# Kernel tuning notes

Hardware: AMD Instinct MI355X
Metric: run time of the kernel (lower is better)

## Reference

```python
import jax, jax.numpy as jnp
import numpy as np

B, D, F_UP, F_DOWN, C = 4096, 768, 12288, 12288, 256


def setup_inputs() -> dict:
    key = jax.random.key(0)
    ks = jax.random.split(key, 12)
    s = np.float32(1.0 / np.sqrt(D))
    return {
        'initial_acts': jax.random.normal(ks[0], (B, D), jnp.float32),
        'x_up': jax.random.normal(ks[1], (B, D), jnp.float32),
        'ln_scale': jax.random.uniform(ks[2], (B,), jnp.float32) + 0.5,
        'W_enc_up': jax.random.normal(ks[3], (F_UP, D), jnp.float32) * s,
        'b_enc_up': jax.random.normal(ks[4], (F_UP,), jnp.float32) * 0.01,
        'b_dec_up': jax.random.normal(ks[5], (D,), jnp.float32) * 0.01,
        'W_dec_up': jax.random.normal(ks[6], (D, F_UP), jnp.float32) * s,
        'W_enc_down': jax.random.normal(ks[7], (F_DOWN, D), jnp.float32) * s,
        'b_enc_down': jax.random.normal(ks[8], (F_DOWN,), jnp.float32) * 0.01,
        'b_dec_down': jax.random.normal(ks[9], (D,), jnp.float32) * 0.01,
        'W_dec_down': jax.random.normal(ks[10], (D, F_DOWN), jnp.float32) * s,
        'connections': jax.random.randint(ks[11], (F_DOWN, C), 0, F_UP, jnp.int64),
        'k_up': 64,
        'k_down': 64,
    }


def _topk_sparse(pre, k):
    # pre: [B, F] -> keep top-k per row, zeros elsewhere
    vals, idx = jax.lax.top_k(pre, k)
    rows = jnp.arange(pre.shape[0])[:, None]
    return jnp.zeros_like(pre).at[rows, idx].set(vals)


def _topk_encode(x, W_enc, b_enc, b_dec, k):
    # AutoEncoderTopK.encode: relu(encoder(x - b_dec)), then top-k sparsify
    pre = jax.nn.relu((x - b_dec) @ W_enc.T + b_enc)
    return _topk_sparse(pre, k)


def reference(initial_acts, x_up, ln_scale, W_enc_up, b_enc_up, b_dec_up,
              W_dec_up, W_enc_down, b_enc_down, b_dec_down, W_dec_down,
              connections, k_up, k_down):
    f_down, f_up = W_enc_down.shape[0], W_enc_up.shape[0]
    # upstream features (vanilla_forward -> features[up_name])
    feat_up = _topk_encode(x_up, W_enc_up, b_enc_up, b_dec_up, k_up)  # [B, F_up]
    # connection mask [F_down, F_up] from index tensor
    rows = jnp.arange(f_down)[:, None]
    mask = jnp.zeros((f_down, f_up), jnp.bool_).at[rows, connections].set(True)
    # get_pruned_contributions: masked virtual-weight matmul
    virtual_w = (W_enc_down @ W_dec_up) * mask                        # [F_down, F_up]
    contributions = feat_up @ virtual_w.T + (W_enc_down @ b_dec_up)   # [B, F_down]
    # get_initial_contributions + accumulate
    approx = initial_acts @ W_enc_down.T + contributions
    # layernorm scale, encoder bias, b_dec correction
    approx = approx / ln_scale[:, None] + b_enc_down - (W_enc_down @ b_dec_down)
    # downstream TopK + decode
    feat_down = _topk_sparse(approx, k_down)                          # [B, F_down]
    recon = feat_down @ W_dec_down.T + b_dec_down                     # [B, D]
    return recon
```

## Files before the change

kernel.cpp:

```cpp
#include <hip/hip_runtime.h>
#include <stdint.h>

#define B_    4096
#define D_    768
#define FUP   12288
#define FDN   12288
#define CONN  256
#define KTOP  64
#define CHUNK 1024
#define NCH   (B_ / CHUNK)
#define CH2   512
#define NCH2  (B_ / CH2)
#define PDW   1024
#define NPW   (FUP / PDW)

typedef short short8v __attribute__((ext_vector_type(8)));
typedef float f32x4  __attribute__((ext_vector_type(4)));


__device__ __forceinline__ unsigned fkey(float x) {
    unsigned u = __float_as_uint(x);
    return (u & 0x80000000u) ? ~u : (u | 0x80000000u);
}

__device__ void topk64_block(const float* vals, int n, int* gidx, float* gval,
                             unsigned* hist, int* scratch)
{
    const int tid = threadIdx.x;
    if (tid == 0) { scratch[0] = KTOP; scratch[1] = 0; scratch[2] = 0; scratch[3] = 0; }
    for (int l = 24; l >= 0; l -= 8) {
        hist[tid] = 0;
        __syncthreads();
        unsigned prefix = (unsigned)scratch[1];
        unsigned hm = (l == 24) ? 0u : (0xFFFFFFFFu << (l + 8));
        for (int i = tid; i < n; i += 256) {
            unsigned key = fkey(vals[i]);
            if ((key & hm) == (prefix & hm)) atomicAdd(&hist[(key >> l) & 255], 1u);
        }
        __syncthreads();
        if (tid == 0) {
            int need = scratch[0];
            unsigned acc = 0;
            for (int b2 = 255; b2 >= 0; --b2) {
                unsigned h = hist[b2];
                if (acc + h >= (unsigned)need) {
                    scratch[1] = (int)(prefix | ((unsigned)b2 << l));
                    scratch[0] = need - (int)acc;
                    break;
                }
                acc += h;
            }
        }
        __syncthreads();
    }
    unsigned thresh = (unsigned)scratch[1];
    for (int i = tid; i < n; i += 256) {
        float v = vals[i];
        unsigned key = fkey(v);
        if (key > thresh) {
            int p = atomicAdd(&scratch[2], 1);
            gidx[p] = i; gval[p] = v;
        } else if (key == thresh) {
            int p = atomicAdd(&scratch[3], 1);
            if (p < 64) scratch[4 + p] = i;
        }
    }
    __syncthreads();
    if (tid == 0) {
        int cnt = scratch[2];
        int ne  = KTOP - cnt;
        int ec  = scratch[3] < 64 ? scratch[3] : 64;
        for (int a2 = 0; a2 < ne; ++a2) {
            int best = 0x7fffffff, bi = -1;
            for (int q = 0; q < ec; ++q) {
                int id = scratch[4 + q];
                if (id >= 0 && id < best) { best = id; bi = q; }
            }
            if (bi >= 0) {
                scratch[4 + bi] = -1;
                gidx[cnt + a2] = best; gval[cnt + a2] = vals[best];
            }
        }
    }
    __syncthreads();
}


__global__ void k_detect(const int* __restrict__ conn, int* mode) {
    if (blockIdx.x == 0 && threadIdx.x == 0) {
        int z = 1;
        for (int i = 1; i < 128; i += 2) z &= (conn[i] == 0);
        *mode = z;
    }
}

__device__ __forceinline__ int getconn(const int* c, size_t e, int mode) {
    return mode ? c[2 * e] : c[e];
}

__global__ void k_zero(unsigned* __restrict__ p, int n) {
    for (int i = blockIdx.x * blockDim.x + threadIdx.x; i < n;
         i += gridDim.x * blockDim.x)
        p[i] = 0u;
}

__global__ void k_transpose(const float* __restrict__ in, float* __restrict__ out,
                            int R, int Cc) {
    __shared__ float t[32][33];
    int x = blockIdx.x * 32 + threadIdx.x;
    int yb = blockIdx.y * 32;
    for (int j = threadIdx.y; j < 32; j += 8)
        t[j][threadIdx.x] = in[(size_t)(yb + j) * Cc + x];
    __syncthreads();
    int xo  = yb + threadIdx.x;
    int yb2 = blockIdx.x * 32;
    for (int j = threadIdx.y; j < 32; j += 8)
        out[(size_t)(yb2 + j) * R + xo] = t[threadIdx.x][j];
}

__global__ void k_precompute(const float* __restrict__ Wup, const float* __restrict__ Wdn,
                             const float* __restrict__ b_enc_up, const float* __restrict__ b_enc_down,
                             const float* __restrict__ b_dec_up, const float* __restrict__ b_dec_down,
                             float* __restrict__ bias_up, float* __restrict__ c_in,
                             float* __restrict__ c_out) {
    int wave = threadIdx.x >> 6, lane = threadIdx.x & 63;
    int f = blockIdx.x * 4 + wave;
    if (f >= FUP) return;
    const float* ru = Wup + (size_t)f * D_;
    const float* rd = Wdn + (size_t)f * D_;
    float s1 = 0.f, s2 = 0.f, s3 = 0.f;
    for (int d = lane; d < D_; d += 64) {
        float bu = b_dec_up[d], bd = b_dec_down[d];
        s1 += ru[d] * bu;
        float w = rd[d];
        s2 += w * bu;
        s3 += w * bd;
    }
    for (int m = 32; m; m >>= 1) {
        s1 += __shfl_xor(s1, m);
        s2 += __shfl_xor(s2, m);
        s3 += __shfl_xor(s3, m);
    }
    if (!lane) {
        bias_up[f] = b_enc_up[f] - s1;
        c_in[f]  = s2;
        c_out[f] = b_enc_down[f] - s3;
    }
}

__device__ __forceinline__ unsigned short bf16rne(float f) {
    unsigned u = __float_as_uint(f);
    unsigned r = u + 0x7FFFu + ((u >> 16) & 1u);
    return (unsigned short)(r >> 16);
}
__global__ __launch_bounds__(256) void k_split3(const float* __restrict__ in,
                                                unsigned short* __restrict__ out,
                                                int R) {
    const size_t plane = (size_t)R * D_;
    size_t base = ((size_t)blockIdx.x * 256 + threadIdx.x) * 8;
    float v[8];
    *(float4*)&v[0] = *(const float4*)(in + base);
    *(float4*)&v[4] = *(const float4*)(in + base + 4);
    unsigned short h[8], m[8], l[8];
#pragma unroll
    for (int i = 0; i < 8; ++i) {
        float f = v[i];
        unsigned short hb = bf16rne(f);
        float hf = __uint_as_float((unsigned)hb << 16);
        float r1 = f - hf;
        unsigned short mb = bf16rne(r1);
        float mf = __uint_as_float((unsigned)mb << 16);
        float r2 = r1 - mf;
        unsigned short lb = bf16rne(r2);
        h[i] = hb; m[i] = mb; l[i] = lb;
    }
    *(short8v*)(out + base)             = *(short8v*)h;
    *(short8v*)(out + plane + base)     = *(short8v*)m;
    *(short8v*)(out + 2 * plane + base) = *(short8v*)l;
}

#define GBM 128
#define GBN 128
#define GBK 32
#define LDK 40
__global__ __launch_bounds__(256, 2) void k_gemm_mfma(
    const unsigned short* __restrict__ Asp, const unsigned short* __restrict__ Bsp,
    float* __restrict__ C, const float* __restrict__ bias,
    int M, int N, int doRelu)
{
    __shared__ __attribute__((aligned(16))) unsigned short Al[3][GBM][LDK];
    __shared__ __attribute__((aligned(16))) unsigned short Bl[3][GBN][LDK];
    const int tid = threadIdx.x;
    const int bm = blockIdx.y * GBM, bn = blockIdx.x * GBN;
    const int wid = tid >> 6, lane = tid & 63;
    const int wm = (wid >> 1) * 64, wn = (wid & 1) * 64;
    const int l15 = lane & 15, lk8 = (lane >> 4) * 8;
    const size_t psA = (size_t)M * D_, psB = (size_t)N * D_;
    f32x4 acc[4][4] = {};
    for (int k0 = 0; k0 < D_; k0 += GBK) {
        __syncthreads();
#pragma unroll
        for (int t = 0; t < 6; ++t) {
            int id = t * 256 + tid;
            int p = id / 512, rem = id & 511;
            int r = rem >> 2, c4 = rem & 3;
            *(short8v*)&Al[p][r][c4 * 8] =
                *(const short8v*)(Asp + p * psA + (size_t)(bm + r) * D_ + k0 + c4 * 8);
            *(short8v*)&Bl[p][r][c4 * 8] =
                *(const short8v*)(Bsp + p * psB + (size_t)(bn + r) * D_ + k0 + c4 * 8);
        }
        __syncthreads();
        short8v af[3][4], bf[3][4];
#pragma unroll
        for (int i = 0; i < 4; ++i) {
#pragma unroll
            for (int p = 0; p < 3; ++p) {
                af[p][i] = *(const short8v*)&Al[p][wm + i * 16 + l15][lk8];
                bf[p][i] = *(const short8v*)&Bl[p][wn + i * 16 + l15][lk8];
            }
        }
#pragma unroll
        for (int i = 0; i < 4; ++i)
#pragma unroll
            for (int j = 0; j < 4; ++j) {
                acc[i][j] = __builtin_amdgcn_mfma_f32_16x16x32_bf16(af[0][i], bf[0][j], acc[i][j], 0, 0, 0);
                acc[i][j] = __builtin_amdgcn_mfma_f32_16x16x32_bf16(af[0][i], bf[1][j], acc[i][j], 0, 0, 0);
                acc[i][j] = __builtin_amdgcn_mfma_f32_16x16x32_bf16(af[1][i], bf[0][j], acc[i][j], 0, 0, 0);
                acc[i][j] = __builtin_amdgcn_mfma_f32_16x16x32_bf16(af[1][i], bf[1][j], acc[i][j], 0, 0, 0);
                acc[i][j] = __builtin_amdgcn_mfma_f32_16x16x32_bf16(af[0][i], bf[2][j], acc[i][j], 0, 0, 0);
                acc[i][j] = __builtin_amdgcn_mfma_f32_16x16x32_bf16(af[2][i], bf[0][j], acc[i][j], 0, 0, 0);
            }
    }
#pragma unroll
    for (int i = 0; i < 4; ++i) {
        int gr0 = bm + wm + i * 16 + (lane >> 4) * 4;
#pragma unroll
        for (int j = 0; j < 4; ++j) {
            int gc = bn + wn + j * 16 + l15;
            float bv = bias ? bias[gc] : 0.f;
#pragma unroll
            for (int q = 0; q < 4; ++q) {
                float v = acc[i][j][q] + bv;
                if (doRelu) v = fmaxf(v, 0.f);
                C[(size_t)(gr0 + q) * N + gc] = v;
            }
        }
    }
}

__global__ __launch_bounds__(256) void k_topk_up(const float* __restrict__ big,
                                                 int* __restrict__ up_idx,
                                                 float* __restrict__ up_val) {
    __shared__ __attribute__((aligned(16))) float row[FUP];
    __shared__ unsigned hist[256];
    __shared__ int scratch[68];
    int b = blockIdx.x;
    const float4* s4 = (const float4*)(big + (size_t)b * FUP);
    float4* r4 = (float4*)row;
    for (int i = threadIdx.x; i < FUP / 4; i += 256) r4[i] = s4[i];
    __syncthreads();
    topk64_block(row, FUP, up_idx + b * 64, up_val + b * 64, hist, scratch);
}

__global__ __launch_bounds__(256) void k_sortwin(
    const int* __restrict__ conn, const int* __restrict__ mode_p,
    unsigned short* __restrict__ ent_fu, unsigned char* __restrict__ ent_c,
    unsigned short* __restrict__ woff)
{
    __shared__ int crow[CONN];
    __shared__ int cnt[NPW + 1];
    __shared__ int base[NPW + 1];
    __shared__ int cur[NPW + 1];
    int fd = blockIdx.x, tid = threadIdx.x;
    int mode = *mode_p;
    crow[tid] = getconn(conn, (size_t)fd * CONN + tid, mode);
    if (tid <= NPW) cnt[tid] = 0;
    __syncthreads();
    int fu = crow[tid];
    bool dup = false;
    for (int q = 0; q < tid; ++q) dup |= (crow[q] == fu);
    int win = dup ? NPW : (fu / PDW);
    atomicAdd(&cnt[win], 1);
    __syncthreads();
    if (tid == 0) {
        int run = 0;
        for (int i = 0; i <= NPW; ++i) { base[i] = run; run += cnt[i]; }
    }
    __syncthreads();
    if (tid <= NPW) {
        woff[fd * (NPW + 2) + tid] = (unsigned short)base[tid];
        cur[tid] = base[tid];
    }
    if (tid == 0) woff[fd * (NPW + 2) + NPW + 1] = (unsigned short)CONN;
    __syncthreads();
    int pos = atomicAdd(&cur[win], 1);
    ent_fu[(size_t)fd * CONN + pos] = (unsigned short)fu;
    ent_c[(size_t)fd * CONN + pos]  = (unsigned char)tid;
}

__global__ __launch_bounds__(256) void k_pd2(
    const float* __restrict__ Wdn, const float* __restrict__ WduT,
    const unsigned short* __restrict__ ent_fu, const unsigned char* __restrict__ ent_c,
    const unsigned short* __restrict__ woff, float* __restrict__ pd)
{
    __shared__ __attribute__((aligned(16))) float wrow[D_];
    int fd = blockIdx.x, win = blockIdx.y, tid = threadIdx.x;
    int s = woff[fd * (NPW + 2) + win];
    int e = woff[fd * (NPW + 2) + win + 1];
    if (win == NPW) {
        for (int t = s + tid; t < e; t += 256)
            pd[(size_t)fd * CONN + ent_c[(size_t)fd * CONN + t]] = 0.f;
        return;
    }
    if (s == e) return;
    const float4* wsrc = (const float4*)(Wdn + (size_t)fd * D_);
    for (int i = tid; i < D_ / 4; i += 256) ((float4*)wrow)[i] = wsrc[i];
    __syncthreads();
    const int wave = tid >> 6, lane = tid & 63;
    const int grp = lane >> 4, gi = lane & 15;
    float4 wr[12];
#pragma unroll
    for (int j = 0; j < 12; ++j)
        wr[j] = *(const float4*)&wrow[gi * 4 + j * 64];
    for (int q = s + wave * 4; q < e; q += 16) {
        int idx = q + grp;
        bool act = idx < e;
        int idxc = act ? idx : (e - 1);
        int fu = ent_fu[(size_t)fd * CONN + idxc];
        const float* wu = WduT + (size_t)fu * D_;
        float sacc = 0.f;
#pragma unroll
        for (int j = 0; j < 12; ++j) {
            float4 u = *(const float4*)&wu[gi * 4 + j * 64];
            sacc = fmaf(u.x, wr[j].x, sacc);
            sacc = fmaf(u.y, wr[j].y, sacc);
            sacc = fmaf(u.z, wr[j].z, sacc);
            sacc = fmaf(u.w, wr[j].w, sacc);
        }
#pragma unroll
        for (int m = 1; m < 16; m <<= 1) sacc += __shfl_xor(sacc, m);
        if (act && gi == 0)
            pd[(size_t)fd * CONN + ent_c[(size_t)fd * CONN + idx]] = sacc;
    }
}

__global__ void k_hist(const int* __restrict__ conn, const int* __restrict__ mode_p,
                       unsigned* __restrict__ counts, int total) {
    int mode = *mode_p;
    for (int e = blockIdx.x * blockDim.x + threadIdx.x; e < total;
         e += gridDim.x * blockDim.x)
        atomicAdd(&counts[getconn(conn, (size_t)e, mode)], 1u);
}

__global__ void k_scan(const unsigned* __restrict__ counts,
                       unsigned* __restrict__ offsets, unsigned* __restrict__ cursor) {
    __shared__ unsigned sums[256];
    int tid = threadIdx.x;
    const int CH = FUP / 256;
    unsigned local = 0;
    for (int i = 0; i < CH; ++i) local += counts[tid * CH + i];
    sums[tid] = local;
    __syncthreads();
    for (int off = 1; off < 256; off <<= 1) {
        unsigned v = 0;
        if (tid >= off) v = sums[tid - off];
        __syncthreads();
        sums[tid] += v;
        __syncthreads();
    }
    unsigned run = (tid == 0) ? 0u : sums[tid - 1];
    for (int i = 0; i < CH; ++i) {
        int idx = tid * CH + i;
        offsets[idx] = run;
        cursor[idx]  = run;
        run += counts[idx];
    }
    if (tid == 255) offsets[FUP] = run;
}

__global__ void k_scatter(const int* __restrict__ conn, const int* __restrict__ mode_p,
                          const float* __restrict__ pd, unsigned* __restrict__ cursor,
                          unsigned short* __restrict__ rev_fd, float* __restrict__ rev_w,
                          int total) {
    int mode = *mode_p;
    for (int e = blockIdx.x * blockDim.x + threadIdx.x; e < total;
         e += gridDim.x * blockDim.x) {
        int fu = getconn(conn, (size_t)e, mode);
        unsigned pos = atomicAdd(&cursor[fu], 1u);
        rev_fd[pos] = (unsigned short)(e >> 8);
        rev_w[pos]  = pd[e];
    }
}

__global__ __launch_bounds__(256) void k_down(
    const float* __restrict__ big , const float* __restrict__ ln_scale,
    const float* __restrict__ c_in, const float* __restrict__ c_out,
    const int* __restrict__ up_idx, const float* __restrict__ up_val,
    const unsigned* __restrict__ offsets, const unsigned short* __restrict__ rev_fd,
    const float* __restrict__ rev_w, int* __restrict__ down_idx,
    float* __restrict__ down_val)
{
    __shared__ __attribute__((aligned(16))) float contrib[FDN];
    __shared__ unsigned hist[256];
    __shared__ int scratch[68];
    int b = blockIdx.x, tid = threadIdx.x;
    float4* c4 = (float4*)contrib;
    for (int i = tid; i < FDN / 4; i += 256) c4[i] = make_float4(0.f, 0.f, 0.f, 0.f);
    __syncthreads();
    for (int j = 0; j < KTOP; ++j) {
        int fu = up_idx[b * 64 + j];
        float v = up_val[b * 64 + j];
        unsigned s = offsets[fu], e = offsets[fu + 1];
        for (unsigned t = s + tid; t < e; t += 256)
            atomicAdd(&contrib[rev_fd[t]], v * rev_w[t]);
    }
    __syncthreads();
    float ls = ln_scale[b];
    const float* ap = big + (size_t)b * FDN;
    for (int i = tid; i < FDN; i += 256)
        contrib[i] = (ap[i] + contrib[i] + c_in[i]) / ls + c_out[i];
    __syncthreads();
    topk64_block(contrib, FDN, down_idx + b * 64, down_val + b * 64, hist, scratch);
}

__global__ __launch_bounds__(256) void k_decode(
    const int* __restrict__ down_idx, const float* __restrict__ down_val,
    const float* __restrict__ WddT, const float* __restrict__ b_dec_down,
    float* __restrict__ out)
{
    __shared__ int fidx[64];
    __shared__ float fval[64];
    int b = blockIdx.x, tid = threadIdx.x;
    if (tid < 64) { fidx[tid] = down_idx[b * 64 + tid]; fval[tid] = down_val[b * 64 + tid]; }
    __syncthreads();
    float a0 = b_dec_down[tid], a1 = b_dec_down[tid + 256], a2 = b_dec_down[tid + 512];
    for (int j = 0; j < 64; ++j) {
        const float* r = WddT + (size_t)fidx[j] * D_;
        float v = fval[j];
        a0 += v * r[tid];
        a1 += v * r[tid + 256];
        a2 += v * r[tid + 512];
    }
    float* o = out + (size_t)b * D_;
    o[tid] = a0; o[tid + 256] = a1; o[tid + 512] = a2;
}


extern "C" void kernel_launch(void* const* d_in, const int* in_sizes, int n_in,
                              void* d_out, int out_size, void* d_ws, size_t ws_size,
                              hipStream_t stream)
{
    const float* initial_acts = (const float*)d_in[0];
    const float* x_up         = (const float*)d_in[1];
    const float* ln_scale     = (const float*)d_in[2];
    const float* W_enc_up     = (const float*)d_in[3];
    const float* b_enc_up     = (const float*)d_in[4];
    const float* b_dec_up     = (const float*)d_in[5];
    const float* W_dec_up     = (const float*)d_in[6];
    const float* W_enc_down   = (const float*)d_in[7];
    const float* b_enc_down   = (const float*)d_in[8];
    const float* b_dec_down   = (const float*)d_in[9];
    const float* W_dec_down   = (const float*)d_in[10];
    const int*   conn         = (const int*)d_in[11];
    float* out = (float*)d_out;

    char* w = (char*)d_ws;
    float*          big      = (float*)(w);
    float*          pd       = (float*)(w);
    unsigned short* ent_fu   = (unsigned short*)(w + 12582912);
    unsigned char*  ent_c    = (unsigned char*) (w + 18874368);
    unsigned short* woff     = (unsigned short*)(w + 22020096);
    unsigned short* Bsplit   = (unsigned short*)(w + 50331648);
    float*          Wt       = (float*)(w + 50331648);
    float*          rev_w    = (float*)(w + 106954752);
    unsigned short* Asplit1  = (unsigned short*)(w + 106954752);
    unsigned short* rev_fd   = (unsigned short*)(w + 119537664);
    unsigned short* Asplit2  = (unsigned short*)(w + 125829120);
    int*            up_idx   = (int*)  (w + 128188416);
    float*          up_val   = (float*)(w + 129236992);
    int*            down_idx = (int*)  (w + 130285568);
    float*          down_val = (float*)(w + 131334144);
    unsigned*       offsets  = (unsigned*)(w + 132382720);
    unsigned*       cursor   = (unsigned*)(w + 132448256);
    unsigned*       counts   = (unsigned*)(w + 132513792);
    float*          bias_up  = (float*)(w + 132579328);
    float*          c_in     = (float*)(w + 132628480);
    float*          c_out    = (float*)(w + 132677632);
    int*            mode_p   = (int*)  (w + 132726784);

    const int total_conn = FDN * CONN;
    dim3 tb(32, 8);

    k_detect<<<1, 64, 0, stream>>>(conn, mode_p);
    k_precompute<<<FUP / 4, 256, 0, stream>>>(W_enc_up, W_enc_down, b_enc_up, b_enc_down,
                                              b_dec_up, b_dec_down, bias_up, c_in, c_out);
    k_split3<<<FUP * D_ / 2048, 256, 0, stream>>>(W_enc_up, Bsplit, FUP);
    for (int c = 0; c < NCH; ++c) {
        k_split3<<<CHUNK * D_ / 2048, 256, 0, stream>>>(x_up + (size_t)c * CHUNK * D_,
                                                        Asplit1, CHUNK);
        k_gemm_mfma<<<dim3(FUP / GBN, CHUNK / GBM), 256, 0, stream>>>(
            Asplit1, Bsplit, big, bias_up, CHUNK, FUP, 1);
        k_topk_up<<<CHUNK, 256, 0, stream>>>(big, up_idx + (size_t)c * CHUNK * 64,
                                             up_val + (size_t)c * CHUNK * 64);
    }
    k_transpose<<<dim3(FUP / 32, D_ / 32), tb, 0, stream>>>(W_dec_up, Wt, D_, FUP);
    k_sortwin<<<FDN, 256, 0, stream>>>(conn, mode_p, ent_fu, ent_c, woff);
    k_pd2<<<dim3(FDN, NPW + 1), 256, 0, stream>>>(W_enc_down, Wt, ent_fu, ent_c, woff, pd);
    k_zero<<<48, 256, 0, stream>>>(counts, FUP);
    k_hist<<<4096, 256, 0, stream>>>(conn, mode_p, counts, total_conn);
    k_scan<<<1, 256, 0, stream>>>(counts, offsets, cursor);
    k_scatter<<<4096, 256, 0, stream>>>(conn, mode_p, pd, cursor, rev_fd, rev_w, total_conn);
    k_split3<<<FDN * D_ / 2048, 256, 0, stream>>>(W_enc_down, Bsplit, FDN);
    for (int c = 0; c < NCH2; ++c) {
        k_split3<<<CH2 * D_ / 2048, 256, 0, stream>>>(initial_acts + (size_t)c * CH2 * D_,
                                                      Asplit2, CH2);
        k_gemm_mfma<<<dim3(FDN / GBN, CH2 / GBM), 256, 0, stream>>>(
            Asplit2, Bsplit, big, nullptr, CH2, FDN, 0);
        k_down<<<CH2, 256, 0, stream>>>(big, ln_scale + (size_t)c * CH2, c_in, c_out,
                                        up_idx + (size_t)c * CH2 * 64,
                                        up_val + (size_t)c * CH2 * 64,
                                        offsets, rev_fd, rev_w,
                                        down_idx + (size_t)c * CH2 * 64,
                                        down_val + (size_t)c * CH2 * 64);
    }
    k_transpose<<<dim3(FDN / 32, D_ / 32), tb, 0, stream>>>(W_dec_down, Wt, D_, FDN);
    k_decode<<<B_, 256, 0, stream>>>(down_idx, down_val, Wt, b_dec_down, out);
}
```

Before: 3.982 ms.

## Load GEMM tiles directly into LDS with XOR swizzle and grouped block remap

Replaces register-staged global-to-LDS copies in the split-bf16 MFMA GEMM with global_load_lds direct transfers, and precomputes per-thread source and destination pointers outside the k-loop. The padded LDS layout gives way to an unpadded layout with an XOR swizzle on the 16-byte column chunk, meant to avoid bank conflicts on fragment reads. Workgroup IDs are also remapped in groups of eight, probably to improve L2 locality across blocks. This removes VGPR staging and padding, but depends on the swizzle matching the direct-load destination ordering.

```diff
diff --git a/kernel.cpp b/kernel.cpp
--- a/kernel.cpp
+++ b/kernel.cpp
@@ -182,43 +182,69 @@
 #define GBM 128
 #define GBN 128
 #define GBK 32
-#define LDK 40
+
+__device__ __forceinline__ void gld16(const void* g, void* l) {
+    __builtin_amdgcn_global_load_lds(
+        (const __attribute__((address_space(1))) unsigned int*)g,
+        (__attribute__((address_space(3))) unsigned int*)l, 16, 0, 0);
+}
+
 __global__ __launch_bounds__(256, 2) void k_gemm_mfma(
     const unsigned short* __restrict__ Asp, const unsigned short* __restrict__ Bsp,
     float* __restrict__ C, const float* __restrict__ bias,
     int M, int N, int doRelu)
 {
-    __shared__ __attribute__((aligned(16))) unsigned short Al[3][GBM][LDK];
-    __shared__ __attribute__((aligned(16))) unsigned short Bl[3][GBN][LDK];
+    __shared__ __attribute__((aligned(16))) unsigned short L[3072 * 8];
     const int tid = threadIdx.x;
-    const int bm = blockIdx.y * GBM, bn = blockIdx.x * GBN;
+    const int nbx = gridDim.x;
+    const int nwg = nbx * gridDim.y;
+    int id = blockIdx.y * nbx + blockIdx.x;
+    if ((nwg & 7) == 0) id = (id & 7) * (nwg >> 3) + (id >> 3);
+    const int bm = (id / nbx) * GBM, bn = (id % nbx) * GBN;
+
     const int wid = tid >> 6, lane = tid & 63;
     const int wm = (wid >> 1) * 64, wn = (wid & 1) * 64;
-    const int l15 = lane & 15, lk8 = (lane >> 4) * 8;
+    const int l15 = lane & 15, g4 = lane >> 4;
     const size_t psA = (size_t)M * D_, psB = (size_t)N * D_;
+
+    const unsigned short* gsrc[12];
+    unsigned short* ldst[12];
+#pragma unroll
+    for (int q2 = 0; q2 < 12; ++q2) {
+        int s  = wid * 768 + q2 * 64 + lane;
+        int isB = (s >= 1536);
+        int sl = isB ? (s - 1536) : s;
+        int p  = sl >> 9;
+        int rem = sl & 511;
+        int r  = rem >> 2;
+        int cs = rem & 3;
+        int c  = cs ^ ((r >> 1) & 3);
+        const unsigned short* bp = isB ? Bsp : Asp;
+        size_t ps = isB ? psB : psA;
+        int row = (isB ? bn : bm) + r;
+        gsrc[q2] = bp + (size_t)p * ps + (size_t)row * D_ + c * 8;
+        ldst[q2] = L + (wid * 768 + q2 * 64) * 8;
+    }
+    const int fA = ((wm + l15) >> 1) & 3;
+    const int fB = ((wn + l15) >> 1) & 3;
+    const unsigned short* aB = L + (wm + l15) * 32 + ((g4 ^ fA) * 8);
+    const unsigned short* bB = L + 1536 * 8 + (wn + l15) * 32 + ((g4 ^ fB) * 8);
+
     f32x4 acc[4][4] = {};
     for (int k0 = 0; k0 < D_; k0 += GBK) {
         __syncthreads();
 #pragma unroll
-        for (int t = 0; t < 6; ++t) {
-            int id = t * 256 + tid;
-            int p = id / 512, rem = id & 511;
-            int r = rem >> 2, c4 = rem & 3;
-            *(short8v*)&Al[p][r][c4 * 8] =
-                *(const short8v*)(Asp + p * psA + (size_t)(bm + r) * D_ + k0 + c4 * 8);
-            *(short8v*)&Bl[p][r][c4 * 8] =
-                *(const short8v*)(Bsp + p * psB + (size_t)(bn + r) * D_ + k0 + c4 * 8);
-        }
+        for (int q2 = 0; q2 < 12; ++q2)
+            gld16(gsrc[q2] + k0, ldst[q2]);
         __syncthreads();
         short8v af[3][4], bf[3][4];
 #pragma unroll
-        for (int i = 0; i < 4; ++i) {
+        for (int i = 0; i < 4; ++i)
 #pragma unroll
             for (int p = 0; p < 3; ++p) {
-                af[p][i] = *(const short8v*)&Al[p][wm + i * 16 + l15][lk8];
-                bf[p][i] = *(const short8v*)&Bl[p][wn + i * 16 + l15][lk8];
+                af[p][i] = *(const short8v*)(aB + p * 4096 + i * 512);
+                bf[p][i] = *(const short8v*)(bB + p * 4096 + i * 512);
             }
-        }
 #pragma unroll
         for (int i = 0; i < 4; ++i)
 #pragma unroll
```

Measured after the change: 3.886 ms. 2.4% less time.
